# Performance work log

Hardware: AMD Instinct MI355X
Metric: run time of the kernel (lower is better)

Reference implementation:

```python
import jax, jax.numpy as jnp
import numpy as np

KH = KW = 3  # kernel_size

def _extract_patches(x):
    # x: [B, C, H, W] -> patches [B, C, Ho, Wo, KH*KW], same ordering as nn.Unfold
    B, C, H, W = x.shape
    Ho, Wo = H - KH + 1, W - KW + 1
    slices = [x[:, :, i:i + Ho, j:j + Wo] for i in range(KH) for j in range(KW)]
    return jnp.stack(slices, axis=-1)

def setup_inputs() -> dict:
    key = jax.random.key(0)
    k1, k2 = jax.random.split(key)
    x = jax.random.normal(k1, (16, 64, 128, 128), dtype=jnp.float32)
    W = jax.random.normal(k2, (8, KH * KW), dtype=jnp.float32) * (1.0 / np.sqrt(KH * KW))
    return {"x": x, "W": W}

def reference(x, W):
    # per-patch: out = Linear(SiLU(patch)) for each of n_convs kernels and each channel
    B, C, H, Wd = x.shape
    Ho, Wo = H - KH + 1, Wd - KW + 1
    patches = _extract_patches(x)                      # [B, C, Ho, Wo, 9]
    act = jax.nn.silu(patches)
    # out channel ordering: kern + channel * n_convs -> [B, C, K, Ho, Wo]
    out = jnp.einsum('bchwj,kj->bckhw', act, W)
    return out.reshape(B, C * W.shape[0], Ho, Wo)
```

## Files before the change

kernel.cpp:

```cpp
#include <hip/hip_runtime.h>

#define B_   16
#define C_   64
#define H_   128
#define W_   128
#define HO   126
#define WO   126
#define NK   8
#define ROWS 14
#define INR  16

__global__ __launch_bounds__(256) void conv_silu_kernel(
    const float* __restrict__ x, const float* __restrict__ Wt,
    float* __restrict__ out)
{
    __shared__ float s[INR][W_];

    const int band = blockIdx.x;
    const int c    = blockIdx.y;
    const int b    = blockIdx.z;
    const int tid  = threadIdx.x;
    const int ho0  = band * ROWS;

    float w[NK * 9];
#pragma unroll
    for (int i = 0; i < NK * 9; ++i) w[i] = Wt[i];

    const float4* xv = (const float4*)(x + ((size_t)(b * C_ + c) * H_ + ho0) * W_);
#pragma unroll
    for (int i = 0; i < 2; ++i) {
        const int f   = tid + i * 256;
        const float4 v = xv[f];
        const int row = f >> 5;
        const int col = (f & 31) << 2;
        const float vs[4] = {v.x, v.y, v.z, v.w};
#pragma unroll
        for (int q = 0; q < 4; ++q) {
            const float t = vs[q];
            s[row][col + q] = t * __builtin_amdgcn_rcpf(1.0f + __expf(-t));
        }
    }
    __syncthreads();

    const int wo = tid & 127;
    const int ty = tid >> 7;
    if (wo >= WO) return;

    float* op = out + ((size_t)(b * (C_ * NK) + c * NK) * HO + ho0) * WO;

#pragma unroll
    for (int it = 0; it < ROWS / 2; ++it) {
        const int r = it * 2 + ty;
        const float a0 = s[r    ][wo], a1 = s[r    ][wo + 1], a2 = s[r    ][wo + 2];
        const float a3 = s[r + 1][wo], a4 = s[r + 1][wo + 1], a5 = s[r + 1][wo + 2];
        const float a6 = s[r + 2][wo], a7 = s[r + 2][wo + 1], a8 = s[r + 2][wo + 2];
#pragma unroll
        for (int k = 0; k < NK; ++k) {
            const float acc = w[k*9+0]*a0 + w[k*9+1]*a1 + w[k*9+2]*a2
                            + w[k*9+3]*a3 + w[k*9+4]*a4 + w[k*9+5]*a5
                            + w[k*9+6]*a6 + w[k*9+7]*a7 + w[k*9+8]*a8;
            op[((size_t)k * HO + r) * WO + wo] = acc;
        }
    }
}

extern "C" void kernel_launch(void* const* d_in, const int* in_sizes, int n_in,
                              void* d_out, int out_size, void* d_ws, size_t ws_size,
                              hipStream_t stream) {
    const float* x  = (const float*)d_in[0];
    const float* Wt = (const float*)d_in[1];
    float* out = (float*)d_out;

    dim3 grid(9, C_, B_);
    conv_silu_kernel<<<grid, 256, 0, stream>>>(x, Wt, out);
}
```

Measured before the change: 126.5 us.

## Assign one output kernel per wavefront with register sliding window over rows

The block grows to 512 threads, and each of the 8 wavefronts now computes a single output kernel using 9 weights held in registers, instead of every thread computing all 8 kernels with 72 weights. Each lane handles two output columns and walks down the 14 rows, reusing a 3x3 register window so only one new row is read from shared memory per step. The input tile is loaded with one float4 per thread and written to shared memory as a float4. This is meant to cut register pressure and LDS traffic. In exchange it doubles the threads per block and adds a wrapped column index for the second half.

```diff
diff --git a/kernel.cpp b/kernel.cpp
--- a/kernel.cpp
+++ b/kernel.cpp
@@ -10,7 +10,7 @@
 #define ROWS 14
 #define INR  16
 
-__global__ __launch_bounds__(256) void conv_silu_kernel(
+__global__ __launch_bounds__(512) void conv_silu_kernel(
     const float* __restrict__ x, const float* __restrict__ Wt,
     float* __restrict__ out)
 {
@@ -22,44 +22,69 @@
     const int tid  = threadIdx.x;
     const int ho0  = band * ROWS;
 
-    float w[NK * 9];
-#pragma unroll
-    for (int i = 0; i < NK * 9; ++i) w[i] = Wt[i];
-
-    const float4* xv = (const float4*)(x + ((size_t)(b * C_ + c) * H_ + ho0) * W_);
-#pragma unroll
-    for (int i = 0; i < 2; ++i) {
-        const int f   = tid + i * 256;
-        const float4 v = xv[f];
-        const int row = f >> 5;
-        const int col = (f & 31) << 2;
-        const float vs[4] = {v.x, v.y, v.z, v.w};
-#pragma unroll
-        for (int q = 0; q < 4; ++q) {
-            const float t = vs[q];
-            s[row][col + q] = t * __builtin_amdgcn_rcpf(1.0f + __expf(-t));
-        }
+    {
+        const float4* xv =
+            (const float4*)(x + ((size_t)(b * C_ + c) * H_ + ho0) * W_);
+        const float4 v = xv[tid];
+        const int row = tid >> 5;
+        const int col = (tid & 31) << 2;
+        float4 sv;
+        sv.x = v.x * __builtin_amdgcn_rcpf(1.0f + __expf(-v.x));
+        sv.y = v.y * __builtin_amdgcn_rcpf(1.0f + __expf(-v.y));
+        sv.z = v.z * __builtin_amdgcn_rcpf(1.0f + __expf(-v.z));
+        sv.w = v.w * __builtin_amdgcn_rcpf(1.0f + __expf(-v.w));
+        *(float4*)&s[row][col] = sv;
     }
     __syncthreads();
 
-    const int wo = tid & 127;
-    const int ty = tid >> 7;
-    if (wo >= WO) return;
+    const int l  = tid & 63;
+    const int ws = __builtin_amdgcn_readfirstlane((int)(threadIdx.x >> 6));
 
-    float* op = out + ((size_t)(b * (C_ * NK) + c * NK) * HO + ho0) * WO;
+    float w9[9];
+#pragma unroll
+    for (int j = 0; j < 9; ++j) w9[j] = Wt[ws * 9 + j];
+
+    float* op = out + ((size_t)((b * C_ + c) * NK + ws) * HO + ho0) * WO;
+
+    float tA[3][3], tB[3][3];
+#pragma unroll
+    for (int j = 0; j < 3; ++j) {
+#pragma unroll
+        for (int d = 0; d < 3; ++d) {
+            tA[j][d] = s[j][l + d];
+            tB[j][d] = s[j][(64 + l + d) & 127];
+        }
+    }
 
 #pragma unroll
-    for (int it = 0; it < ROWS / 2; ++it) {
-        const int r = it * 2 + ty;
-        const float a0 = s[r    ][wo], a1 = s[r    ][wo + 1], a2 = s[r    ][wo + 2];
-        const float a3 = s[r + 1][wo], a4 = s[r + 1][wo + 1], a5 = s[r + 1][wo + 2];
-        const float a6 = s[r + 2][wo], a7 = s[r + 2][wo + 1], a8 = s[r + 2][wo + 2];
+    for (int r = 0; r < ROWS; ++r) {
+        float accA = 0.f, accB = 0.f;
 #pragma unroll
-        for (int k = 0; k < NK; ++k) {
-            const float acc = w[k*9+0]*a0 + w[k*9+1]*a1 + w[k*9+2]*a2
-                            + w[k*9+3]*a3 + w[k*9+4]*a4 + w[k*9+5]*a5
-                            + w[k*9+6]*a6 + w[k*9+7]*a7 + w[k*9+8]*a8;
-            op[((size_t)k * HO + r) * WO + wo] = acc;
+        for (int j = 0; j < 3; ++j) {
+#pragma unroll
+            for (int d = 0; d < 3; ++d) {
+                const float ww = w9[j * 3 + d];
+                accA += ww * tA[j][d];
+                accB += ww * tB[j][d];
+            }
+        }
+        op[r * WO + l] = accA;
+        if (l < 62) op[r * WO + 64 + l] = accB;
+
+        if (r < ROWS - 1) {
+#pragma unroll
+            for (int j = 0; j < 2; ++j) {
+#pragma unroll
+                for (int d = 0; d < 3; ++d) {
+                    tA[j][d] = tA[j + 1][d];
+                    tB[j][d] = tB[j + 1][d];
+                }
+            }
+#pragma unroll
+            for (int d = 0; d < 3; ++d) {
+                tA[2][d] = s[r + 3][l + d];
+                tB[2][d] = s[r + 3][(64 + l + d) & 127];
+            }
         }
     }
 }
@@ -72,5 +97,5 @@
     float* out = (float*)d_out;
 
     dim3 grid(9, C_, B_);
-    conv_silu_kernel<<<grid, 256, 0, stream>>>(x, Wt, out);
+    conv_silu_kernel<<<grid, 512, 0, stream>>>(x, Wt, out);
 }
```

Result: faster. 116.6 us, median of 2 (-7.9%).
